# Performance work log

Hardware: AMD Instinct MI355X
Metric: run time of the kernel (lower is better)

The kernel has to match this reference:

```python
import jax, jax.numpy as jnp
import numpy as np

V, E, H, T, B, NT = 50000, 100, 256, 128, 512, 20


def _gl(k, shape, fan):
    return jax.random.normal(k, shape, jnp.float32) * (1.0 / np.sqrt(fan))


def setup_inputs() -> dict:
    key = jax.random.key(0)
    ks = jax.random.split(key, 20)
    inp = {
        'word_inputs': jax.random.randint(ks[0], (B, T), 0, V),
        'word_seq_lengths': jnp.full((B,), T, dtype=jnp.int32),
        'char_inputs': jnp.zeros((B * T, 1), dtype=jnp.int32),
        'batch_label': jax.random.randint(ks[1], (B, T), 0, NT),
        'mask': jnp.ones((B, T), dtype=jnp.bool_),
        'embed': _gl(ks[2], (V, E), E).at[0].set(0.0),  # padding_idx=0
    }
    i = 3
    for d in ('f', 'b'):
        inp['Wih_' + d] = _gl(ks[i + 0], (4 * H, E), E)
        inp['Whh_' + d] = _gl(ks[i + 1], (4 * H, H), H)
        inp['bih_' + d] = jnp.zeros((4 * H,), jnp.float32)
        inp['bhh_' + d] = jnp.zeros((4 * H,), jnp.float32)
        inp['Q_' + d] = _gl(ks[i + 2], (H, E), H)  # mogrify round 1: x <- 2*sig(h Q) * x
        inp['R_' + d] = _gl(ks[i + 3], (E, H), E)  # mogrify round 2: h <- 2*sig(x R) * h
        i += 4
    inp['Wt'] = _gl(ks[i], (NT, 2 * H), 2 * H)
    inp['bt'] = jnp.zeros((NT,), jnp.float32)
    return inp


def _mog_lstm(xs, Wih, Whh, bih, bhh, Q, R):
    # xs: [T, B, E]; mog=2 Mogrifier rounds then standard LSTM cell (i,f,g,o order)
    def step(carry, xt):
        h, c = carry
        xm = 2.0 * jax.nn.sigmoid(h @ Q) * xt
        hm = 2.0 * jax.nn.sigmoid(xm @ R) * h
        g = xm @ Wih.T + hm @ Whh.T + (bih + bhh)
        gi, gf, gg, go = jnp.split(g, 4, axis=-1)
        c = jax.nn.sigmoid(gf) * c + jax.nn.sigmoid(gi) * jnp.tanh(gg)
        h = jax.nn.sigmoid(go) * jnp.tanh(c)
        return (h, c), h
    h0 = jnp.zeros((xs.shape[1], H), xs.dtype)
    _, hs = jax.lax.scan(step, (h0, h0), xs)
    return hs  # [T, B, H]


def reference(word_inputs, word_seq_lengths, char_inputs, batch_label, mask,
              embed, Wih_f, Whh_f, bih_f, bhh_f, Q_f, R_f,
              Wih_b, Whh_b, bih_b, bhh_b, Q_b, R_b, Wt, bt):
    x = embed[word_inputs]                       # [B, T, E]; dropout = identity (eval)
    xs = jnp.transpose(x, (1, 0, 2))             # [T, B, E]
    hf = _mog_lstm(xs, Wih_f, Whh_f, bih_f, bhh_f, Q_f, R_f)
    hb = _mog_lstm(xs[::-1], Wih_b, Whh_b, bih_b, bhh_b, Q_b, R_b)[::-1]
    feat = jnp.concatenate([hf, hb], axis=-1)    # [T, B, 2H]
    logits = feat @ Wt.T + bt                    # [T, B, NT]
    tag_seq = jnp.argmax(logits, axis=-1).T      # [B, T]
    return mask.astype(tag_seq.dtype) * tag_seq
```

## Files before the change

kernel.cpp:

```cpp
#include <hip/hip_runtime.h>
#include <math.h>

#define TT 128
#define BB 512
#define EE 100
#define HH 256
#define G4 1024
#define NTAG 20
#define KP 368
#define PWPSZ (KP * G4)
#define QPSZ  25600
#define RPSZ  28672

__device__ __forceinline__ float sigm(float x) { return 1.0f / (1.0f + expf(-x)); }

__global__ void prep6(const float* __restrict__ Wih, const float* __restrict__ Whh,
                      const float* __restrict__ bih, const float* __restrict__ bhh,
                      const float* __restrict__ Q, const float* __restrict__ R,
                      float* __restrict__ PWp, float* __restrict__ QP,
                      float* __restrict__ RP, float* __restrict__ bP)
{
    int idx = blockIdx.x * blockDim.x + threadIdx.x;
    if (idx < PWPSZ) {
        int k = idx >> 10, n = idx & 1023;
        PWp[idx] = (k < EE) ? Wih[n * EE + k]
                 : (k < EE + HH) ? Whh[n * HH + (k - EE)] : 0.f;
    } else if (idx < PWPSZ + QPSZ) {
        int i = idx - PWPSZ;
        int kq = i / 400, rem = i - kq * 400;
        int e = rem >> 2, kk = rem & 3;
        QP[i] = Q[(kq * 4 + kk) * EE + e];
    } else if (idx < PWPSZ + QPSZ + RPSZ) {
        int i = idx - (PWPSZ + QPSZ);
        int kq = i >> 10, rem = i & 1023;
        int j = rem >> 2, kk = rem & 3;
        int k = kq * 4 + kk;
        RP[i] = (k < EE) ? R[k * HH + j] : 0.f;
    } else if (idx < PWPSZ + QPSZ + RPSZ + G4) {
        int n = idx - (PWPSZ + QPSZ + RPSZ);
        bP[n] = bih[n] + bhh[n];
    }
}

#define P1L(S, kq) { \
    q##S = *(const float4*)(QP + (kq) * 400 + e * 4); \
    h##S = *(const float4*)(sH + r1 * HH + (kq) * 4); }
#define P1F(S) { a0 += (h##S).x*(q##S).x + (h##S).y*(q##S).y + (h##S).z*(q##S).z + (h##S).w*(q##S).w; }

#define P2L(S, kq) { \
    r##S = *(const float4*)(RP + (kq) * 1024 + j2 * 4); \
    X##S##0 = *(const float4*)(sA + r20 * KP + (kq) * 4); \
    X##S##1 = *(const float4*)(sA + r21 * KP + (kq) * 4); }
#define P2F(S) { \
    s0 += (X##S##0).x*(r##S).x + (X##S##0).y*(r##S).y + (X##S##0).z*(r##S).z + (X##S##0).w*(r##S).w; \
    s1 += (X##S##1).x*(r##S).x + (X##S##1).y*(r##S).y + (X##S##1).z*(r##S).z + (X##S##1).w*(r##S).w; }

#define P3L(S, kk) { const int kc_ = ((kk) <= 364) ? (kk) : 364; \
    const float* wp_ = PW + (size_t)kc_ * G4 + n0; \
    W##S##0 = *(const float4*)(wp_);        W##S##1 = *(const float4*)(wp_ + G4); \
    W##S##2 = *(const float4*)(wp_ + 2*G4); W##S##3 = *(const float4*)(wp_ + 3*G4); \
    const float* xp_ = sA + rg3 * KP + kc_; \
    X##S##0 = *(const float4*)(xp_);        X##S##1 = *(const float4*)(xp_ + KP); }
#define P3F(S) { \
    a00 += (X##S##0).x*(W##S##0).x + (X##S##0).y*(W##S##1).x + (X##S##0).z*(W##S##2).x + (X##S##0).w*(W##S##3).x; \
    a01 += (X##S##0).x*(W##S##0).y + (X##S##0).y*(W##S##1).y + (X##S##0).z*(W##S##2).y + (X##S##0).w*(W##S##3).y; \
    a02 += (X##S##0).x*(W##S##0).z + (X##S##0).y*(W##S##1).z + (X##S##0).z*(W##S##2).z + (X##S##0).w*(W##S##3).z; \
    a03 += (X##S##0).x*(W##S##0).w + (X##S##0).y*(W##S##1).w + (X##S##0).z*(W##S##2).w + (X##S##0).w*(W##S##3).w; \
    a10 += (X##S##1).x*(W##S##0).x + (X##S##1).y*(W##S##1).x + (X##S##1).z*(W##S##2).x + (X##S##1).w*(W##S##3).x; \
    a11 += (X##S##1).x*(W##S##0).y + (X##S##1).y*(W##S##1).y + (X##S##1).z*(W##S##2).y + (X##S##1).w*(W##S##3).y; \
    a12 += (X##S##1).x*(W##S##0).z + (X##S##1).y*(W##S##1).z + (X##S##1).z*(W##S##2).z + (X##S##1).w*(W##S##3).z; \
    a13 += (X##S##1).x*(W##S##0).w + (X##S##1).y*(W##S##1).w + (X##S##1).z*(W##S##2).w + (X##S##1).w*(W##S##3).w; }

__global__ __launch_bounds__(512, 1) void lstm6(
    const int* __restrict__ words, const float* __restrict__ embed,
    const float* __restrict__ QPf, const float* __restrict__ RPf,
    const float* __restrict__ PWf, const float* __restrict__ bPf,
    const float* __restrict__ QPb, const float* __restrict__ RPb,
    const float* __restrict__ PWb, const float* __restrict__ bPb,
    float* hfbuf, float* hbbuf)
{
    const int bid = blockIdx.x;
    const int dir = bid & 1;
    const int cb  = bid >> 1;
    const int b0  = cb * 4;
    const int tid = threadIdx.x;

    const float* QP = dir ? QPb : QPf;
    const float* RP = dir ? RPb : RPf;
    const float* PW = dir ? PWb : PWf;
    const float* bP = dir ? bPb : bPf;
    float* hout = dir ? hbbuf : hfbuf;

    __shared__ alignas(16) float sA[4 * KP];
    __shared__ alignas(16) float sH[4 * HH];
    __shared__ alignas(16) float sG[4 * G4];
    __shared__ int sWords[4 * TT];

    const int e  = tid & 127;
    const int r1 = tid >> 7;
    const int j2  = tid & 255;
    const int r20 = (tid >> 8) * 2, r21 = r20 + 1;
    const int n0  = (tid & 255) * 4;
    const int rg3 = (tid >> 8) * 2;
    const int j4  = tid & 255;
    const int r4a = (tid >> 8) * 2, r4b = r4a + 1;
    float c0 = 0.f, c1 = 0.f;

    const float4 bv = *(const float4*)(bP + n0);

    sWords[tid & 511] = words[(b0 + (tid >> 7)) * TT + (tid & 127)];
    if (tid < 48) {
        const int r = tid / 12, p = tid - r * 12;
        sA[r * KP + 356 + p] = 0.f;
    }
    __syncthreads();

    for (int s = 0; s < TT; ++s) {
        const int t = dir ? (TT - 1 - s) : s;

        if (e < EE) {
            const int w = sWords[r1 * TT + t];
            const float x = __builtin_nontemporal_load(&embed[(size_t)w * EE + e]);
            if (s == 0) {
                sA[r1 * KP + e] = x;
            } else {
                float a0 = 0.f;
                float4 qA, qB, qC, qD, hA, hB, hC, hD;
                P1L(A,0); P1L(B,1); P1L(C,2); P1L(D,3);
                for (int kb = 0; kb <= 56; kb += 4) {
                    P1F(A); P1L(A, kb+4); P1F(B); P1L(B, kb+5);
                    P1F(C); P1L(C, kb+6); P1F(D); P1L(D, kb+7);
                }
                P1F(A); P1F(B); P1F(C); P1F(D);
                sA[r1 * KP + e] = 2.f * sigm(a0) * x;
            }
        }
        __syncthreads();

        if (s == 0) {
            sA[r20 * KP + EE + j2] = 0.f;
            sA[r21 * KP + EE + j2] = 0.f;
        } else {
            float s0 = 0.f, s1 = 0.f;
            float4 rA, rB, rC, rD;
            float4 XA0, XA1, XB0, XB1, XC0, XC1, XD0, XD1;
            P2L(A,0); P2L(B,1); P2L(C,2); P2L(D,3);
            for (int kb = 0; kb <= 20; kb += 4) {
                P2F(A); P2L(A, kb+4); P2F(B); P2L(B, kb+5);
                P2F(C); P2L(C, kb+6); P2F(D); P2L(D, kb+7);
            }
            P2F(A); P2F(B); P2F(C); P2F(D);
            sA[r20 * KP + EE + j2] = 2.f * sigm(s0) * sH[r20 * HH + j2];
            sA[r21 * KP + EE + j2] = 2.f * sigm(s1) * sH[r21 * HH + j2];
        }
        __syncthreads();

        {
            float a00=bv.x,a01=bv.y,a02=bv.z,a03=bv.w;
            float a10=bv.x,a11=bv.y,a12=bv.z,a13=bv.w;
            float4 WA0,WA1,WA2,WA3,XA0,XA1, WB0,WB1,WB2,WB3,XB0,XB1;
            float4 WC0,WC1,WC2,WC3,XC0,XC1, WD0,WD1,WD2,WD3,XD0,XD1;
            P3L(A,0); P3L(B,4); P3L(C,8); P3L(D,12);
            for (int kb = 0; kb <= 344; kb += 16) {
                P3F(A); P3L(A, kb+16); P3F(B); P3L(B, kb+20);
                P3F(C); P3L(C, kb+24); P3F(D); P3L(D, kb+28);
            }
            P3F(A); P3F(B);
            *(float4*)(sG + (rg3 + 0) * G4 + n0) = make_float4(a00,a01,a02,a03);
            *(float4*)(sG + (rg3 + 1) * G4 + n0) = make_float4(a10,a11,a12,a13);
        }
        __syncthreads();

        {
            const float gi0 = sG[r4a*G4 + j4],       gi1 = sG[r4b*G4 + j4];
            const float gf0 = sG[r4a*G4 + 256 + j4], gf1 = sG[r4b*G4 + 256 + j4];
            const float gg0 = sG[r4a*G4 + 512 + j4], gg1 = sG[r4b*G4 + 512 + j4];
            const float go0 = sG[r4a*G4 + 768 + j4], go1 = sG[r4b*G4 + 768 + j4];
            c0 = sigm(gf0) * c0 + sigm(gi0) * tanhf(gg0);
            c1 = sigm(gf1) * c1 + sigm(gi1) * tanhf(gg1);
            const float h0 = sigm(go0) * tanhf(c0);
            const float h1 = sigm(go1) * tanhf(c1);
            sH[r4a * HH + j4] = h0;
            sH[r4b * HH + j4] = h1;
            __builtin_nontemporal_store(h0, &hout[((size_t)t * BB + b0 + r4a) * HH + j4]);
            __builtin_nontemporal_store(h1, &hout[((size_t)t * BB + b0 + r4b) * HH + j4]);
        }
        __syncthreads();
    }
}

__global__ __launch_bounds__(256) void logits_kernel(
    const float* __restrict__ hf, const float* __restrict__ hb,
    const float* __restrict__ Wt, const float* __restrict__ bt,
    int* __restrict__ out)
{
    __shared__ float sW[NTAG][2 * HH];
    __shared__ float sb[NTAG];
    const int tid = threadIdx.x;
    for (int i = tid; i < NTAG * 2 * HH; i += 256) (&sW[0][0])[i] = Wt[i];
    if (tid < NTAG) sb[tid] = bt[tid];
    __syncthreads();

    const int pos = blockIdx.x * 256 + tid;
    const int b  = pos & 511;
    const int t0 = pos >> 9;
    const int t1 = t0 + 64;

    float acc0[NTAG], acc1[NTAG];
    #pragma unroll
    for (int n = 0; n < NTAG; ++n) { acc0[n] = sb[n]; acc1[n] = sb[n]; }

    const float* f0 = hf + ((size_t)t0 * BB + b) * HH;
    const float* f1 = hf + ((size_t)t1 * BB + b) * HH;
    for (int k = 0; k < HH; k += 4) {
        const float4 a0 = *(const float4*)(f0 + k);
        const float4 a1 = *(const float4*)(f1 + k);
        #pragma unroll
        for (int n = 0; n < NTAG; ++n) {
            const float4 w = *(const float4*)&sW[n][k];
            acc0[n] += a0.x * w.x + a0.y * w.y + a0.z * w.z + a0.w * w.w;
            acc1[n] += a1.x * w.x + a1.y * w.y + a1.z * w.z + a1.w * w.w;
        }
    }
    const float* g0 = hb + ((size_t)t0 * BB + b) * HH;
    const float* g1 = hb + ((size_t)t1 * BB + b) * HH;
    for (int k = 0; k < HH; k += 4) {
        const float4 a0 = *(const float4*)(g0 + k);
        const float4 a1 = *(const float4*)(g1 + k);
        #pragma unroll
        for (int n = 0; n < NTAG; ++n) {
            const float4 w = *(const float4*)&sW[n][HH + k];
            acc0[n] += a0.x * w.x + a0.y * w.y + a0.z * w.z + a0.w * w.w;
            acc1[n] += a1.x * w.x + a1.y * w.y + a1.z * w.z + a1.w * w.w;
        }
    }

    float b0v = acc0[0]; int i0 = 0;
    float b1v = acc1[0]; int i1 = 0;
    #pragma unroll
    for (int n = 1; n < NTAG; ++n) {
        if (acc0[n] > b0v) { b0v = acc0[n]; i0 = n; }
        if (acc1[n] > b1v) { b1v = acc1[n]; i1 = n; }
    }
    out[b * TT + t0] = i0;
    out[b * TT + t1] = i1;
}

extern "C" void kernel_launch(void* const* d_in, const int* in_sizes, int n_in,
                              void* d_out, int out_size, void* d_ws, size_t ws_size,
                              hipStream_t stream)
{
    (void)in_sizes; (void)n_in; (void)out_size; (void)ws_size;

    const int*   words = (const int*)  d_in[0];
    const float* embd  = (const float*)d_in[5];
    const float* Wih_f = (const float*)d_in[6];
    const float* Whh_f = (const float*)d_in[7];
    const float* bih_f = (const float*)d_in[8];
    const float* bhh_f = (const float*)d_in[9];
    const float* Q_f   = (const float*)d_in[10];
    const float* R_f   = (const float*)d_in[11];
    const float* Wih_b = (const float*)d_in[12];
    const float* Whh_b = (const float*)d_in[13];
    const float* bih_b = (const float*)d_in[14];
    const float* bhh_b = (const float*)d_in[15];
    const float* Q_b   = (const float*)d_in[16];
    const float* R_b   = (const float*)d_in[17];
    const float* Wt    = (const float*)d_in[18];
    const float* bt    = (const float*)d_in[19];
    int* out = (int*)d_out;

    float* ws   = (float*)d_ws;
    float* PW_f = ws;
    float* QP_f = PW_f + PWPSZ;
    float* RP_f = QP_f + QPSZ;
    float* bP_f = RP_f + RPSZ;
    float* PW_b = bP_f + G4;
    float* QP_b = PW_b + PWPSZ;
    float* RP_b = QP_b + QPSZ;
    float* bP_b = RP_b + RPSZ;
    float* hf   = bP_b + G4;
    float* hb   = hf + (size_t)TT * BB * HH;

    const int prep_grid = (PWPSZ + QPSZ + RPSZ + G4 + 255) / 256;
    prep6<<<prep_grid, 256, 0, stream>>>(Wih_f, Whh_f, bih_f, bhh_f, Q_f, R_f,
                                         PW_f, QP_f, RP_f, bP_f);
    prep6<<<prep_grid, 256, 0, stream>>>(Wih_b, Whh_b, bih_b, bhh_b, Q_b, R_b,
                                         PW_b, QP_b, RP_b, bP_b);
    lstm6<<<256, 512, 0, stream>>>(words, embd, QP_f, RP_f, PW_f, bP_f,
                                   QP_b, RP_b, PW_b, bP_b, hf, hb);
    logits_kernel<<<128, 256, 0, stream>>>(hf, hb, Wt, bt, out);
}
```

Before: 3.995 ms.

## Split gate GEMM over K between thread halves with 4-row register tiles and interleaved weights

The gate matmul now splits the K dimension (input plus hidden) into two halves handled by the two thread groups. Each thread computes all 4 batch rows for 4 gate columns, so every weight load is reused four times instead of twice. Weights are repacked into a k-chunk-interleaved layout that lets a thread read 16 contiguous floats, and activations are stored transposed so one float4 holds all four rows. The partial sums go to a doubled shared buffer and are added during the cell update. The Q and R mogrifier loops are also repacked for 16-float contiguous loads with split accumulators. The cost is more shared memory, an extra reduction read per gate, and higher register pressure.

```diff
diff --git a/kernel.cpp b/kernel.cpp
--- a/kernel.cpp
+++ b/kernel.cpp
@@ -7,71 +7,71 @@
 #define HH 256
 #define G4 1024
 #define NTAG 20
-#define KP 368
-#define PWPSZ (KP * G4)
-#define QPSZ  25600
-#define RPSZ  28672
+#define NCH 92
+#define PW3SZ (NCH * 4096)
+#define QP2SZ (16 * 1600)
+#define RP3SZ (7 * 4096)
 
 __device__ __forceinline__ float sigm(float x) { return 1.0f / (1.0f + expf(-x)); }
 
-__global__ void prep6(const float* __restrict__ Wih, const float* __restrict__ Whh,
+__global__ void prep7(const float* __restrict__ Wih, const float* __restrict__ Whh,
                       const float* __restrict__ bih, const float* __restrict__ bhh,
                       const float* __restrict__ Q, const float* __restrict__ R,
-                      float* __restrict__ PWp, float* __restrict__ QP,
-                      float* __restrict__ RP, float* __restrict__ bP)
+                      float* __restrict__ PW3, float* __restrict__ QP2,
+                      float* __restrict__ RP3, float* __restrict__ bP)
 {
     int idx = blockIdx.x * blockDim.x + threadIdx.x;
-    if (idx < PWPSZ) {
-        int k = idx >> 10, n = idx & 1023;
-        PWp[idx] = (k < EE) ? Wih[n * EE + k]
+    if (idx < PW3SZ) {
+        int chunk = idx >> 12, rem = idx & 4095;
+        int n = rem >> 2, kk = rem & 3;
+        int k = chunk * 4 + kk;
+        PW3[idx] = (k < EE) ? Wih[n * EE + k]
                  : (k < EE + HH) ? Whh[n * HH + (k - EE)] : 0.f;
-    } else if (idx < PWPSZ + QPSZ) {
-        int i = idx - PWPSZ;
-        int kq = i / 400, rem = i - kq * 400;
-        int e = rem >> 2, kk = rem & 3;
-        QP[i] = Q[(kq * 4 + kk) * EE + e];
-    } else if (idx < PWPSZ + QPSZ + RPSZ) {
-        int i = idx - (PWPSZ + QPSZ);
-        int kq = i >> 10, rem = i & 1023;
-        int j = rem >> 2, kk = rem & 3;
-        int k = kq * 4 + kk;
-        RP[i] = (k < EE) ? R[k * HH + j] : 0.f;
-    } else if (idx < PWPSZ + QPSZ + RPSZ + G4) {
-        int n = idx - (PWPSZ + QPSZ + RPSZ);
+    } else if (idx < PW3SZ + QP2SZ) {
+        int i = idx - PW3SZ;
+        int kqb = i / 1600, rem = i - kqb * 1600;
+        int e = rem >> 4, q = (rem >> 2) & 3, kk = rem & 3;
+        int k = (kqb * 4 + q) * 4 + kk;
+        QP2[i] = Q[k * EE + e];
+    } else if (idx < PW3SZ + QP2SZ + RP3SZ) {
+        int i = idx - (PW3SZ + QP2SZ);
+        int kqb = i >> 12, rem = i & 4095;
+        int j = rem >> 4, q = (rem >> 2) & 3, kk = rem & 3;
+        int k = (kqb * 4 + q) * 4 + kk;
+        RP3[i] = (k < EE) ? R[k * HH + j] : 0.f;
+    } else if (idx < PW3SZ + QP2SZ + RP3SZ + G4) {
+        int n = idx - (PW3SZ + QP2SZ + RP3SZ);
         bP[n] = bih[n] + bhh[n];
     }
 }
 
-#define P1L(S, kq) { \
-    q##S = *(const float4*)(QP + (kq) * 400 + e * 4); \
-    h##S = *(const float4*)(sH + r1 * HH + (kq) * 4); }
-#define P1F(S) { a0 += (h##S).x*(q##S).x + (h##S).y*(q##S).y + (h##S).z*(q##S).z + (h##S).w*(q##S).w; }
-
-#define P2L(S, kq) { \
-    r##S = *(const float4*)(RP + (kq) * 1024 + j2 * 4); \
-    X##S##0 = *(const float4*)(sA + r20 * KP + (kq) * 4); \
-    X##S##1 = *(const float4*)(sA + r21 * KP + (kq) * 4); }
-#define P2F(S) { \
-    s0 += (X##S##0).x*(r##S).x + (X##S##0).y*(r##S).y + (X##S##0).z*(r##S).z + (X##S##0).w*(r##S).w; \
-    s1 += (X##S##1).x*(r##S).x + (X##S##1).y*(r##S).y + (X##S##1).z*(r##S).z + (X##S##1).w*(r##S).w; }
-
-#define P3L(S, kk) { const int kc_ = ((kk) <= 364) ? (kk) : 364; \
-    const float* wp_ = PW + (size_t)kc_ * G4 + n0; \
-    W##S##0 = *(const float4*)(wp_);        W##S##1 = *(const float4*)(wp_ + G4); \
-    W##S##2 = *(const float4*)(wp_ + 2*G4); W##S##3 = *(const float4*)(wp_ + 3*G4); \
-    const float* xp_ = sA + rg3 * KP + kc_; \
-    X##S##0 = *(const float4*)(xp_);        X##S##1 = *(const float4*)(xp_ + KP); }
+#define P3L(S, c) { const int cc_ = ((c) <= 45) ? (c) : 45; \
+    const float* wp_ = PWd + (size_t)(cbase + cc_) * 4096 + n0 * 4; \
+    W##S##0 = *(const float4*)(wp_);      W##S##1 = *(const float4*)(wp_ + 4); \
+    W##S##2 = *(const float4*)(wp_ + 8);  W##S##3 = *(const float4*)(wp_ + 12); \
+    const float* xp_ = sAT + (cbase + cc_) * 16; \
+    X##S##0 = *(const float4*)(xp_);      X##S##1 = *(const float4*)(xp_ + 4); \
+    X##S##2 = *(const float4*)(xp_ + 8);  X##S##3 = *(const float4*)(xp_ + 12); }
+
 #define P3F(S) { \
-    a00 += (X##S##0).x*(W##S##0).x + (X##S##0).y*(W##S##1).x + (X##S##0).z*(W##S##2).x + (X##S##0).w*(W##S##3).x; \
-    a01 += (X##S##0).x*(W##S##0).y + (X##S##0).y*(W##S##1).y + (X##S##0).z*(W##S##2).y + (X##S##0).w*(W##S##3).y; \
-    a02 += (X##S##0).x*(W##S##0).z + (X##S##0).y*(W##S##1).z + (X##S##0).z*(W##S##2).z + (X##S##0).w*(W##S##3).z; \
-    a03 += (X##S##0).x*(W##S##0).w + (X##S##0).y*(W##S##1).w + (X##S##0).z*(W##S##2).w + (X##S##0).w*(W##S##3).w; \
-    a10 += (X##S##1).x*(W##S##0).x + (X##S##1).y*(W##S##1).x + (X##S##1).z*(W##S##2).x + (X##S##1).w*(W##S##3).x; \
-    a11 += (X##S##1).x*(W##S##0).y + (X##S##1).y*(W##S##1).y + (X##S##1).z*(W##S##2).y + (X##S##1).w*(W##S##3).y; \
-    a12 += (X##S##1).x*(W##S##0).z + (X##S##1).y*(W##S##1).z + (X##S##1).z*(W##S##2).z + (X##S##1).w*(W##S##3).z; \
-    a13 += (X##S##1).x*(W##S##0).w + (X##S##1).y*(W##S##1).w + (X##S##1).z*(W##S##2).w + (X##S##1).w*(W##S##3).w; }
-
-__global__ __launch_bounds__(512, 1) void lstm6(
+    a00 += (X##S##0).x*(W##S##0).x + (X##S##1).x*(W##S##0).y + (X##S##2).x*(W##S##0).z + (X##S##3).x*(W##S##0).w; \
+    a01 += (X##S##0).x*(W##S##1).x + (X##S##1).x*(W##S##1).y + (X##S##2).x*(W##S##1).z + (X##S##3).x*(W##S##1).w; \
+    a02 += (X##S##0).x*(W##S##2).x + (X##S##1).x*(W##S##2).y + (X##S##2).x*(W##S##2).z + (X##S##3).x*(W##S##2).w; \
+    a03 += (X##S##0).x*(W##S##3).x + (X##S##1).x*(W##S##3).y + (X##S##2).x*(W##S##3).z + (X##S##3).x*(W##S##3).w; \
+    a10 += (X##S##0).y*(W##S##0).x + (X##S##1).y*(W##S##0).y + (X##S##2).y*(W##S##0).z + (X##S##3).y*(W##S##0).w; \
+    a11 += (X##S##0).y*(W##S##1).x + (X##S##1).y*(W##S##1).y + (X##S##2).y*(W##S##1).z + (X##S##3).y*(W##S##1).w; \
+    a12 += (X##S##0).y*(W##S##2).x + (X##S##1).y*(W##S##2).y + (X##S##2).y*(W##S##2).z + (X##S##3).y*(W##S##2).w; \
+    a13 += (X##S##0).y*(W##S##3).x + (X##S##1).y*(W##S##3).y + (X##S##2).y*(W##S##3).z + (X##S##3).y*(W##S##3).w; \
+    a20 += (X##S##0).z*(W##S##0).x + (X##S##1).z*(W##S##0).y + (X##S##2).z*(W##S##0).z + (X##S##3).z*(W##S##0).w; \
+    a21 += (X##S##0).z*(W##S##1).x + (X##S##1).z*(W##S##1).y + (X##S##2).z*(W##S##1).z + (X##S##3).z*(W##S##1).w; \
+    a22 += (X##S##0).z*(W##S##2).x + (X##S##1).z*(W##S##2).y + (X##S##2).z*(W##S##2).z + (X##S##3).z*(W##S##2).w; \
+    a23 += (X##S##0).z*(W##S##3).x + (X##S##1).z*(W##S##3).y + (X##S##2).z*(W##S##3).z + (X##S##3).z*(W##S##3).w; \
+    a30 += (X##S##0).w*(W##S##0).x + (X##S##1).w*(W##S##0).y + (X##S##2).w*(W##S##0).z + (X##S##3).w*(W##S##0).w; \
+    a31 += (X##S##0).w*(W##S##1).x + (X##S##1).w*(W##S##1).y + (X##S##2).w*(W##S##1).z + (X##S##3).w*(W##S##1).w; \
+    a32 += (X##S##0).w*(W##S##2).x + (X##S##1).w*(W##S##2).y + (X##S##2).w*(W##S##2).z + (X##S##3).w*(W##S##2).w; \
+    a33 += (X##S##0).w*(W##S##3).x + (X##S##1).w*(W##S##3).y + (X##S##2).w*(W##S##3).z + (X##S##3).w*(W##S##3).w; }
+
+__global__ __launch_bounds__(512, 1) void lstm7(
     const int* __restrict__ words, const float* __restrict__ embed,
     const float* __restrict__ QPf, const float* __restrict__ RPf,
     const float* __restrict__ PWf, const float* __restrict__ bPf,
@@ -85,33 +85,37 @@
     const int b0  = cb * 4;
     const int tid = threadIdx.x;
 
-    const float* QP = dir ? QPb : QPf;
-    const float* RP = dir ? RPb : RPf;
-    const float* PW = dir ? PWb : PWf;
-    const float* bP = dir ? bPb : bPf;
+    const float* QPd = dir ? QPb : QPf;
+    const float* RPd = dir ? RPb : RPf;
+    const float* PWd = dir ? PWb : PWf;
+    const float* bP  = dir ? bPb : bPf;
     float* hout = dir ? hbbuf : hfbuf;
 
-    __shared__ alignas(16) float sA[4 * KP];
+    __shared__ alignas(16) float sAT[368 * 4];
+    __shared__ alignas(16) float sAlin[4 * 112];
     __shared__ alignas(16) float sH[4 * HH];
-    __shared__ alignas(16) float sG[4 * G4];
+    __shared__ alignas(16) float sG[2 * 4 * G4];
     __shared__ int sWords[4 * TT];
 
     const int e  = tid & 127;
     const int r1 = tid >> 7;
     const int j2  = tid & 255;
     const int r20 = (tid >> 8) * 2, r21 = r20 + 1;
-    const int n0  = (tid & 255) * 4;
-    const int rg3 = (tid >> 8) * 2;
+    const int n0    = (tid & 255) * 4;
+    const int g3    = tid >> 8;
+    const int cbase = g3 * 46;
     const int j4  = tid & 255;
     const int r4a = (tid >> 8) * 2, r4b = r4a + 1;
     float c0 = 0.f, c1 = 0.f;
 
-    const float4 bv = *(const float4*)(bP + n0);
+    const float4 bvr = *(const float4*)(bP + n0);
+    const float4 bv  = (g3 == 0) ? bvr : make_float4(0.f, 0.f, 0.f, 0.f);
 
     sWords[tid & 511] = words[(b0 + (tid >> 7)) * TT + (tid & 127)];
-    if (tid < 48) {
-        const int r = tid / 12, p = tid - r * 12;
-        sA[r * KP + 356 + p] = 0.f;
+    if (tid < 48)  sAT[(356 + (tid >> 2)) * 4 + (tid & 3)] = 0.f;
+    if (tid >= 64 && tid < 112) {
+        const int i = tid - 64, r = i / 12, p = i - r * 12;
+        sAlin[r * 112 + 100 + p] = 0.f;
     }
     __syncthreads();
 
@@ -122,60 +126,104 @@
             const int w = sWords[r1 * TT + t];
             const float x = __builtin_nontemporal_load(&embed[(size_t)w * EE + e]);
             if (s == 0) {
-                sA[r1 * KP + e] = x;
+                sAT[e * 4 + r1] = x;
+                sAlin[r1 * 112 + e] = x;
             } else {
-                float a0 = 0.f;
-                float4 qA, qB, qC, qD, hA, hB, hC, hD;
-                P1L(A,0); P1L(B,1); P1L(C,2); P1L(D,3);
-                for (int kb = 0; kb <= 56; kb += 4) {
-                    P1F(A); P1L(A, kb+4); P1F(B); P1L(B, kb+5);
-                    P1F(C); P1L(C, kb+6); P1F(D); P1L(D, kb+7);
+                float ac0 = 0.f, ac1 = 0.f, ac2 = 0.f, ac3 = 0.f;
+                const float* hp0 = sH + r1 * HH;
+                #pragma unroll
+                for (int kqb = 0; kqb < 16; ++kqb) {
+                    const float* qp = QPd + kqb * 1600 + e * 16;
+                    const float4 q0 = *(const float4*)(qp);
+                    const float4 q1 = *(const float4*)(qp + 4);
+                    const float4 q2 = *(const float4*)(qp + 8);
+                    const float4 q3 = *(const float4*)(qp + 12);
+                    const float4 h0 = *(const float4*)(hp0 + kqb * 16);
+                    const float4 h1 = *(const float4*)(hp0 + kqb * 16 + 4);
+                    const float4 h2 = *(const float4*)(hp0 + kqb * 16 + 8);
+                    const float4 h3 = *(const float4*)(hp0 + kqb * 16 + 12);
+                    ac0 += h0.x*q0.x + h0.y*q0.y + h0.z*q0.z + h0.w*q0.w;
+                    ac1 += h1.x*q1.x + h1.y*q1.y + h1.z*q1.z + h1.w*q1.w;
+                    ac2 += h2.x*q2.x + h2.y*q2.y + h2.z*q2.z + h2.w*q2.w;
+                    ac3 += h3.x*q3.x + h3.y*q3.y + h3.z*q3.z + h3.w*q3.w;
                 }
-                P1F(A); P1F(B); P1F(C); P1F(D);
-                sA[r1 * KP + e] = 2.f * sigm(a0) * x;
+                const float xm = 2.f * sigm((ac0 + ac1) + (ac2 + ac3)) * x;
+                sAT[e * 4 + r1] = xm;
+                sAlin[r1 * 112 + e] = xm;
             }
         }
         __syncthreads();
 
         if (s == 0) {
-            sA[r20 * KP + EE + j2] = 0.f;
-            sA[r21 * KP + EE + j2] = 0.f;
+            sAT[(100 + j2) * 4 + r20] = 0.f;
+            sAT[(100 + j2) * 4 + r21] = 0.f;
         } else {
-            float s0 = 0.f, s1 = 0.f;
-            float4 rA, rB, rC, rD;
-            float4 XA0, XA1, XB0, XB1, XC0, XC1, XD0, XD1;
-            P2L(A,0); P2L(B,1); P2L(C,2); P2L(D,3);
-            for (int kb = 0; kb <= 20; kb += 4) {
-                P2F(A); P2L(A, kb+4); P2F(B); P2L(B, kb+5);
-                P2F(C); P2L(C, kb+6); P2F(D); P2L(D, kb+7);
+            float s0a = 0.f, s0b = 0.f, s1a = 0.f, s1b = 0.f;
+            const float* x0p = sAlin + r20 * 112;
+            const float* x1p = sAlin + r21 * 112;
+            #pragma unroll
+            for (int kqb = 0; kqb < 7; ++kqb) {
+                const float* rp = RPd + kqb * 4096 + j2 * 16;
+                const float4 w0 = *(const float4*)(rp);
+                const float4 w1 = *(const float4*)(rp + 4);
+                const float4 w2 = *(const float4*)(rp + 8);
+                const float4 w3 = *(const float4*)(rp + 12);
+                const float4 xa0 = *(const float4*)(x0p + kqb * 16);
+                const float4 xa1 = *(const float4*)(x0p + kqb * 16 + 4);
+                const float4 xa2 = *(const float4*)(x0p + kqb * 16 + 8);
+                const float4 xa3 = *(const float4*)(x0p + kqb * 16 + 12);
+                const float4 xb0 = *(const float4*)(x1p + kqb * 16);
+                const float4 xb1 = *(const float4*)(x1p + kqb * 16 + 4);
+                const float4 xb2 = *(const float4*)(x1p + kqb * 16 + 8);
+                const float4 xb3 = *(const float4*)(x1p + kqb * 16 + 12);
+                s0a += xa0.x*w0.x + xa0.y*w0.y + xa0.z*w0.z + xa0.w*w0.w;
+                s0b += xa1.x*w1.x + xa1.y*w1.y + xa1.z*w1.z + xa1.w*w1.w;
+                s0a += xa2.x*w2.x + xa2.y*w2.y + xa2.z*w2.z + xa2.w*w2.w;
+                s0b += xa3.x*w3.x + xa3.y*w3.y + xa3.z*w3.z + xa3.w*w3.w;
+                s1a += xb0.x*w0.x + xb0.y*w0.y + xb0.z*w0.z + xb0.w*w0.w;
+                s1b += xb1.x*w1.x + xb1.y*w1.y + xb1.z*w1.z + xb1.w*w1.w;
+                s1a += xb2.x*w2.x + xb2.y*w2.y + xb2.z*w2.z + xb2.w*w2.w;
+                s1b += xb3.x*w3.x + xb3.y*w3.y + xb3.z*w3.z + xb3.w*w3.w;
             }
-            P2F(A); P2F(B); P2F(C); P2F(D);
-            sA[r20 * KP + EE + j2] = 2.f * sigm(s0) * sH[r20 * HH + j2];
-            sA[r21 * KP + EE + j2] = 2.f * sigm(s1) * sH[r21 * HH + j2];
+            sAT[(100 + j2) * 4 + r20] = 2.f * sigm(s0a + s0b) * sH[r20 * HH + j2];
+            sAT[(100 + j2) * 4 + r21] = 2.f * sigm(s1a + s1b) * sH[r21 * HH + j2];
         }
         __syncthreads();
 
         {
             float a00=bv.x,a01=bv.y,a02=bv.z,a03=bv.w;
             float a10=bv.x,a11=bv.y,a12=bv.z,a13=bv.w;
-            float4 WA0,WA1,WA2,WA3,XA0,XA1, WB0,WB1,WB2,WB3,XB0,XB1;
-            float4 WC0,WC1,WC2,WC3,XC0,XC1, WD0,WD1,WD2,WD3,XD0,XD1;
-            P3L(A,0); P3L(B,4); P3L(C,8); P3L(D,12);
-            for (int kb = 0; kb <= 344; kb += 16) {
-                P3F(A); P3L(A, kb+16); P3F(B); P3L(B, kb+20);
-                P3F(C); P3L(C, kb+24); P3F(D); P3L(D, kb+28);
+            float a20=bv.x,a21=bv.y,a22=bv.z,a23=bv.w;
+            float a30=bv.x,a31=bv.y,a32=bv.z,a33=bv.w;
+            float4 WA0,WA1,WA2,WA3,XA0,XA1,XA2,XA3;
+            float4 WB0,WB1,WB2,WB3,XB0,XB1,XB2,XB3;
+            float4 WC0,WC1,WC2,WC3,XC0,XC1,XC2,XC3;
+            P3L(A,0); P3L(B,1); P3L(C,2);
+            for (int cc = 0; cc <= 42; cc += 3) {
+                P3F(A); P3L(A, cc+3);
+                P3F(B); P3L(B, cc+4);
+                P3F(C); P3L(C, cc+5);
             }
-            P3F(A); P3F(B);
-            *(float4*)(sG + (rg3 + 0) * G4 + n0) = make_float4(a00,a01,a02,a03);
-            *(float4*)(sG + (rg3 + 1) * G4 + n0) = make_float4(a10,a11,a12,a13);
+            P3F(A);
+            float* sg = sG + g3 * 4096 + n0;
+            *(float4*)(sg)          = make_float4(a00,a01,a02,a03);
+            *(float4*)(sg + G4)     = make_float4(a10,a11,a12,a13);
+            *(float4*)(sg + 2 * G4) = make_float4(a20,a21,a22,a23);
+            *(float4*)(sg + 3 * G4) = make_float4(a30,a31,a32,a33);
         }
         __syncthreads();
 
         {
-            const float gi0 = sG[r4a*G4 + j4],       gi1 = sG[r4b*G4 + j4];
-            const float gf0 = sG[r4a*G4 + 256 + j4], gf1 = sG[r4b*G4 + 256 + j4];
-            const float gg0 = sG[r4a*G4 + 512 + j4], gg1 = sG[r4b*G4 + 512 + j4];
-            const float go0 = sG[r4a*G4 + 768 + j4], go1 = sG[r4b*G4 + 768 + j4];
+            const float* g0 = sG + r4a * G4;
+            const float* g1 = sG + r4b * G4;
+            const float gi0 = g0[j4]       + g0[4096 + j4];
+            const float gf0 = g0[256 + j4] + g0[4096 + 256 + j4];
+            const float gg0 = g0[512 + j4] + g0[4096 + 512 + j4];
+            const float go0 = g0[768 + j4] + g0[4096 + 768 + j4];
+            const float gi1 = g1[j4]       + g1[4096 + j4];
+            const float gf1 = g1[256 + j4] + g1[4096 + 256 + j4];
+            const float gg1 = g1[512 + j4] + g1[4096 + 512 + j4];
+            const float go1 = g1[768 + j4] + g1[4096 + 768 + j4];
             c0 = sigm(gf0) * c0 + sigm(gi0) * tanhf(gg0);
             c1 = sigm(gf1) * c1 + sigm(gi1) * tanhf(gg1);
             const float h0 = sigm(go0) * tanhf(c0);
@@ -272,22 +320,22 @@
 
     float* ws   = (float*)d_ws;
     float* PW_f = ws;
-    float* QP_f = PW_f + PWPSZ;
-    float* RP_f = QP_f + QPSZ;
-    float* bP_f = RP_f + RPSZ;
+    float* QP_f = PW_f + PW3SZ;
+    float* RP_f = QP_f + QP2SZ;
+    float* bP_f = RP_f + RP3SZ;
     float* PW_b = bP_f + G4;
-    float* QP_b = PW_b + PWPSZ;
-    float* RP_b = QP_b + QPSZ;
-    float* bP_b = RP_b + RPSZ;
+    float* QP_b = PW_b + PW3SZ;
+    float* RP_b = QP_b + QP2SZ;
+    float* bP_b = RP_b + RP3SZ;
     float* hf   = bP_b + G4;
     float* hb   = hf + (size_t)TT * BB * HH;
 
-    const int prep_grid = (PWPSZ + QPSZ + RPSZ + G4 + 255) / 256;
-    prep6<<<prep_grid, 256, 0, stream>>>(Wih_f, Whh_f, bih_f, bhh_f, Q_f, R_f,
+    const int prep_grid = (PW3SZ + QP2SZ + RP3SZ + G4 + 255) / 256;
+    prep7<<<prep_grid, 256, 0, stream>>>(Wih_f, Whh_f, bih_f, bhh_f, Q_f, R_f,
                                          PW_f, QP_f, RP_f, bP_f);
-    prep6<<<prep_grid, 256, 0, stream>>>(Wih_b, Whh_b, bih_b, bhh_b, Q_b, R_b,
+    prep7<<<prep_grid, 256, 0, stream>>>(Wih_b, Whh_b, bih_b, bhh_b, Q_b, R_b,
                                          PW_b, QP_b, RP_b, bP_b);
-    lstm6<<<256, 512, 0, stream>>>(words, embd, QP_f, RP_f, PW_f, bP_f,
+    lstm7<<<256, 512, 0, stream>>>(words, embd, QP_f, RP_f, PW_f, bP_f,
                                    QP_b, RP_b, PW_b, bP_b, hf, hb);
     logits_kernel<<<128, 256, 0, stream>>>(hf, hb, Wt, bt, out);
 }
```

After: 4.157 ms. +4.1%, slower.

## Interleave gate columns so each thread computes LSTM cell update directly

Applied to the files above, without the earlier changes.

The packed weight and bias layout is permuted so the four consecutive gate outputs a thread produces are the i,f,g,o values of a single hidden unit. The cell and hidden update can then run straight from registers, which removes the shared gate buffer, its stores and loads, and one block barrier per timestep. The logits kernel also launches twice as many blocks, with each thread handling one timestep instead of two. That raises parallelism but loads the weights into shared memory in more blocks.

```diff
diff --git a/kernel.cpp b/kernel.cpp
--- a/kernel.cpp
+++ b/kernel.cpp
@@ -14,7 +14,7 @@
 
 __device__ __forceinline__ float sigm(float x) { return 1.0f / (1.0f + expf(-x)); }
 
-__global__ void prep6(const float* __restrict__ Wih, const float* __restrict__ Whh,
+__global__ void prep9(const float* __restrict__ Wih, const float* __restrict__ Whh,
                       const float* __restrict__ bih, const float* __restrict__ bhh,
                       const float* __restrict__ Q, const float* __restrict__ R,
                       float* __restrict__ PWp, float* __restrict__ QP,
@@ -22,7 +22,8 @@
 {
     int idx = blockIdx.x * blockDim.x + threadIdx.x;
     if (idx < PWPSZ) {
-        int k = idx >> 10, n = idx & 1023;
+        int k = idx >> 10, p = idx & 1023;
+        int n = (p & 3) * 256 + (p >> 2);
         PWp[idx] = (k < EE) ? Wih[n * EE + k]
                  : (k < EE + HH) ? Whh[n * HH + (k - EE)] : 0.f;
     } else if (idx < PWPSZ + QPSZ) {
@@ -37,8 +38,9 @@
         int k = kq * 4 + kk;
         RP[i] = (k < EE) ? R[k * HH + j] : 0.f;
     } else if (idx < PWPSZ + QPSZ + RPSZ + G4) {
-        int n = idx - (PWPSZ + QPSZ + RPSZ);
-        bP[n] = bih[n] + bhh[n];
+        int p = idx - (PWPSZ + QPSZ + RPSZ);
+        int n = (p & 3) * 256 + (p >> 2);
+        bP[p] = bih[n] + bhh[n];
     }
 }
 
@@ -71,7 +73,7 @@
     a12 += (X##S##1).x*(W##S##0).z + (X##S##1).y*(W##S##1).z + (X##S##1).z*(W##S##2).z + (X##S##1).w*(W##S##3).z; \
     a13 += (X##S##1).x*(W##S##0).w + (X##S##1).y*(W##S##1).w + (X##S##1).z*(W##S##2).w + (X##S##1).w*(W##S##3).w; }
 
-__global__ __launch_bounds__(512, 1) void lstm6(
+__global__ __launch_bounds__(512, 1) void lstm14(
     const int* __restrict__ words, const float* __restrict__ embed,
     const float* __restrict__ QPf, const float* __restrict__ RPf,
     const float* __restrict__ PWf, const float* __restrict__ bPf,
@@ -93,17 +95,15 @@
 
     __shared__ alignas(16) float sA[4 * KP];
     __shared__ alignas(16) float sH[4 * HH];
-    __shared__ alignas(16) float sG[4 * G4];
     __shared__ int sWords[4 * TT];
 
     const int e  = tid & 127;
     const int r1 = tid >> 7;
     const int j2  = tid & 255;
     const int r20 = (tid >> 8) * 2, r21 = r20 + 1;
-    const int n0  = (tid & 255) * 4;
+    const int jj  = tid & 255;
+    const int n0  = jj * 4;
     const int rg3 = (tid >> 8) * 2;
-    const int j4  = tid & 255;
-    const int r4a = (tid >> 8) * 2, r4b = r4a + 1;
     float c0 = 0.f, c1 = 0.f;
 
     const float4 bv = *(const float4*)(bP + n0);
@@ -166,24 +166,14 @@
                 P3F(C); P3L(C, kb+24); P3F(D); P3L(D, kb+28);
             }
             P3F(A); P3F(B);
-            *(float4*)(sG + (rg3 + 0) * G4 + n0) = make_float4(a00,a01,a02,a03);
-            *(float4*)(sG + (rg3 + 1) * G4 + n0) = make_float4(a10,a11,a12,a13);
-        }
-        __syncthreads();
-
-        {
-            const float gi0 = sG[r4a*G4 + j4],       gi1 = sG[r4b*G4 + j4];
-            const float gf0 = sG[r4a*G4 + 256 + j4], gf1 = sG[r4b*G4 + 256 + j4];
-            const float gg0 = sG[r4a*G4 + 512 + j4], gg1 = sG[r4b*G4 + 512 + j4];
-            const float go0 = sG[r4a*G4 + 768 + j4], go1 = sG[r4b*G4 + 768 + j4];
-            c0 = sigm(gf0) * c0 + sigm(gi0) * tanhf(gg0);
-            c1 = sigm(gf1) * c1 + sigm(gi1) * tanhf(gg1);
-            const float h0 = sigm(go0) * tanhf(c0);
-            const float h1 = sigm(go1) * tanhf(c1);
-            sH[r4a * HH + j4] = h0;
-            sH[r4b * HH + j4] = h1;
-            __builtin_nontemporal_store(h0, &hout[((size_t)t * BB + b0 + r4a) * HH + j4]);
-            __builtin_nontemporal_store(h1, &hout[((size_t)t * BB + b0 + r4b) * HH + j4]);
+            c0 = sigm(a01) * c0 + sigm(a00) * tanhf(a02);
+            c1 = sigm(a11) * c1 + sigm(a10) * tanhf(a12);
+            const float h0 = sigm(a03) * tanhf(c0);
+            const float h1 = sigm(a13) * tanhf(c1);
+            sH[rg3 * HH + jj]       = h0;
+            sH[(rg3 + 1) * HH + jj] = h1;
+            __builtin_nontemporal_store(h0, &hout[((size_t)t * BB + b0 + rg3)     * HH + jj]);
+            __builtin_nontemporal_store(h1, &hout[((size_t)t * BB + b0 + rg3 + 1) * HH + jj]);
         }
         __syncthreads();
     }
@@ -202,48 +192,38 @@
     __syncthreads();
 
     const int pos = blockIdx.x * 256 + tid;
-    const int b  = pos & 511;
-    const int t0 = pos >> 9;
-    const int t1 = t0 + 64;
-
-    float acc0[NTAG], acc1[NTAG];
+    const int b = pos & 511;
+    const int t = pos >> 9;
+
+    float acc0[NTAG];
     #pragma unroll
-    for (int n = 0; n < NTAG; ++n) { acc0[n] = sb[n]; acc1[n] = sb[n]; }
-
-    const float* f0 = hf + ((size_t)t0 * BB + b) * HH;
-    const float* f1 = hf + ((size_t)t1 * BB + b) * HH;
+    for (int n = 0; n < NTAG; ++n) acc0[n] = sb[n];
+
+    const float* f0 = hf + ((size_t)t * BB + b) * HH;
     for (int k = 0; k < HH; k += 4) {
         const float4 a0 = *(const float4*)(f0 + k);
-        const float4 a1 = *(const float4*)(f1 + k);
         #pragma unroll
         for (int n = 0; n < NTAG; ++n) {
             const float4 w = *(const float4*)&sW[n][k];
             acc0[n] += a0.x * w.x + a0.y * w.y + a0.z * w.z + a0.w * w.w;
-            acc1[n] += a1.x * w.x + a1.y * w.y + a1.z * w.z + a1.w * w.w;
-        }
-    }
-    const float* g0 = hb + ((size_t)t0 * BB + b) * HH;
-    const float* g1 = hb + ((size_t)t1 * BB + b) * HH;
+        }
+    }
+    const float* g0 = hb + ((size_t)t * BB + b) * HH;
     for (int k = 0; k < HH; k += 4) {
         const float4 a0 = *(const float4*)(g0 + k);
-        const float4 a1 = *(const float4*)(g1 + k);
         #pragma unroll
         for (int n = 0; n < NTAG; ++n) {
             const float4 w = *(const float4*)&sW[n][HH + k];
             acc0[n] += a0.x * w.x + a0.y * w.y + a0.z * w.z + a0.w * w.w;
-            acc1[n] += a1.x * w.x + a1.y * w.y + a1.z * w.z + a1.w * w.w;
         }
     }
 
     float b0v = acc0[0]; int i0 = 0;
-    float b1v = acc1[0]; int i1 = 0;
     #pragma unroll
     for (int n = 1; n < NTAG; ++n) {
         if (acc0[n] > b0v) { b0v = acc0[n]; i0 = n; }
-        if (acc1[n] > b1v) { b1v = acc1[n]; i1 = n; }
-    }
-    out[b * TT + t0] = i0;
-    out[b * TT + t1] = i1;
+    }
+    out[b * TT + t] = i0;
 }
 
 extern "C" void kernel_launch(void* const* d_in, const int* in_sizes, int n_in,
@@ -283,11 +263,11 @@
     float* hb   = hf + (size_t)TT * BB * HH;
 
     const int prep_grid = (PWPSZ + QPSZ + RPSZ + G4 + 255) / 256;
-    prep6<<<prep_grid, 256, 0, stream>>>(Wih_f, Whh_f, bih_f, bhh_f, Q_f, R_f,
+    prep9<<<prep_grid, 256, 0, stream>>>(Wih_f, Whh_f, bih_f, bhh_f, Q_f, R_f,
                                          PW_f, QP_f, RP_f, bP_f);
-    prep6<<<prep_grid, 256, 0, stream>>>(Wih_b, Whh_b, bih_b, bhh_b, Q_b, R_b,
+    prep9<<<prep_grid, 256, 0, stream>>>(Wih_b, Whh_b, bih_b, bhh_b, Q_b, R_b,
                                          PW_b, QP_b, RP_b, bP_b);
-    lstm6<<<256, 512, 0, stream>>>(words, embd, QP_f, RP_f, PW_f, bP_f,
-                                   QP_b, RP_b, PW_b, bP_b, hf, hb);
-    logits_kernel<<<128, 256, 0, stream>>>(hf, hb, Wt, bt, out);
-}
+    lstm14<<<256, 512, 0, stream>>>(words, embd, QP_f, RP_f, PW_f, bP_f,
+                                    QP_b, RP_b, PW_b, bP_b, hf, hb);
+    logits_kernel<<<256, 256, 0, stream>>>(hf, hb, Wt, bt, out);
+}
```

Measured after the change: 3.953 ms. No clear change (-1.0%).
